# Kernel optimization log

Hardware: AMD Instinct MI355X
Metric: run time of the kernel (lower is better)

The kernel has to match this reference:

```python
import jax, jax.numpy as jnp
import numpy as np

GAMMA = 0.1
BUDGET = 64
EPS = 1e-8  # torch cosine_similarity clamp


def setup_inputs() -> dict:
    key = jax.random.key(0)
    k1, k2, k3, k4 = jax.random.split(key, 4)
    num_nodes, feat_dim, num_cand = 100000, 256, 50000
    return {
        "influence_scores": jax.random.normal(k1, (num_cand,), dtype=jnp.float32),
        "node_features": jax.random.normal(k2, (num_nodes, feat_dim), dtype=jnp.float32),
        "candidate_indices": jax.random.randint(k3, (num_cand,), 0, num_nodes, dtype=jnp.int64),
        "injected_feat": jax.random.normal(k4, (feat_dim,), dtype=jnp.float32),
    }


def reference(influence_scores, node_features, candidate_indices, injected_feat):
    # gather candidate features: [num_cand, feat_dim]
    cand_feat = node_features[candidate_indices]
    # cosine similarity vs injected_feat, torch-style eps clamp on norms
    inj_norm = jnp.maximum(jnp.linalg.norm(injected_feat), EPS)
    cand_norm = jnp.maximum(jnp.linalg.norm(cand_feat, axis=-1), EPS)
    sim_penalty = (cand_feat @ injected_feat) / (cand_norm * inj_norm)
    edge_scores = influence_scores - GAMMA * sim_penalty
    top_k = min(BUDGET, candidate_indices.shape[0])
    _, selected_indices = jax.lax.top_k(edge_scores, top_k)
    return candidate_indices[selected_indices], edge_scores
```

## Files before the change

### kernel.cpp

```cpp
#include <hip/hip_runtime.h>
#include <hip/hip_bf16.h>
#include <float.h>
#include <limits.h>

#define FEAT       256
#define GAMMA_F    0.1f
#define EPS_F      1e-8f
#define KSEL       64
#define NBUCK      8192
#define CAP        4096

__device__ __forceinline__ unsigned key_of(float v) {
    unsigned u = __float_as_uint(v);
    return u ^ ((u >> 31) ? 0xFFFFFFFFu : 0x80000000u);
}

__global__ __launch_bounds__(256) void edge_score_kernel(
    const float* __restrict__ infl,
    const float* __restrict__ feats,
    const int*   __restrict__ cand,
    const float* __restrict__ inj,
    float*       __restrict__ scores,
    int num_cand)
{
    const int gtid = blockIdx.x * blockDim.x + threadIdx.x;
    const int wave = gtid >> 6;
    const int lane = threadIdx.x & 63;
    if (wave >= num_cand) return;

    const int row = cand[wave];
    const float4 f = *reinterpret_cast<const float4*>(
        feats + (size_t)row * FEAT + lane * 4);
    const float4 g = *reinterpret_cast<const float4*>(inj + lane * 4);

    float dot = f.x * g.x + f.y * g.y + f.z * g.z + f.w * g.w;
    float nf  = f.x * f.x + f.y * f.y + f.z * f.z + f.w * f.w;
    float ng  = g.x * g.x + g.y * g.y + g.z * g.z + g.w * g.w;

    #pragma unroll
    for (int off = 32; off > 0; off >>= 1) {
        dot += __shfl_xor(dot, off);
        nf  += __shfl_xor(nf, off);
        ng  += __shfl_xor(ng, off);
    }

    if (lane == 0) {
        const float denom = fmaxf(sqrtf(nf), EPS_F) * fmaxf(sqrtf(ng), EPS_F);
        scores[wave] = infl[wave] - GAMMA_F * (dot / denom);
    }
}

__global__ __launch_bounds__(256) void hist_kernel(
    const float* __restrict__ scores,
    unsigned*    __restrict__ hist,
    int n)
{
    __shared__ unsigned h[NBUCK];
    for (int i = threadIdx.x; i < NBUCK; i += 256) h[i] = 0;
    __syncthreads();
    for (int i = blockIdx.x * 256 + threadIdx.x; i < n; i += gridDim.x * 256)
        atomicAdd(&h[key_of(scores[i]) >> 19], 1u);
    __syncthreads();
    for (int i = threadIdx.x; i < NBUCK; i += 256)
        if (h[i]) atomicAdd(&hist[i], h[i]);
}

__global__ __launch_bounds__(256) void scan_kernel(
    const unsigned* __restrict__ hist,
    unsigned*       __restrict__ meta)
{
    __shared__ unsigned csum[256];
    const int t  = threadIdx.x;
    const int hi = NBUCK - 32 * t;
    unsigned s = 0;
    for (int b = hi - 32; b < hi; ++b) s += hist[b];
    csum[t] = s;
    __syncthreads();

    if (t == 0) {
        unsigned cum = 0;
        int tc = 0;
        for (; tc < 256; ++tc) {
            if (cum + csum[tc] >= KSEL) break;
            cum += csum[tc];
        }
        unsigned B = 0;
        if (tc < 256) {
            int b = NBUCK - 32 * tc - 1;
            for (int k = 0; k < 32; ++k, --b) {
                cum += hist[b];
                if (cum >= KSEL) { B = (unsigned)b; break; }
            }
        }
        meta[0] = B;
    }
}

__global__ __launch_bounds__(256) void compact_kernel(
    const float*    __restrict__ scores,
    const unsigned* __restrict__ meta,
    unsigned*       __restrict__ cnt,
    float*          __restrict__ out_v,
    int*            __restrict__ out_i,
    int n)
{
    const unsigned B = meta[0];
    for (int i = blockIdx.x * 256 + threadIdx.x; i < n; i += gridDim.x * 256) {
        const float v = scores[i];
        if ((key_of(v) >> 19) >= B) {
            const unsigned p = atomicAdd(cnt, 1u);
            if (p < CAP) { out_v[p] = v; out_i[p] = i; }
        }
    }
}

__device__ __forceinline__ bool comes_first(float va, int ia, float vb, int ib) {
    return (va > vb) || (va == vb && ia < ib);
}

__global__ __launch_bounds__(256) void final_kernel(
    const unsigned* __restrict__ cnt,
    const float*    __restrict__ in_v,
    const int*      __restrict__ in_i,
    const int*      __restrict__ cand,
    float*          __restrict__ out)
{
    __shared__ float sv[CAP];
    __shared__ int   si[CAP];
    const int t = threadIdx.x;
    const int m = (int)min(*cnt, (unsigned)CAP);

    if (m <= 256) {
        sv[t] = (t < m) ? in_v[t] : -INFINITY;
        si[t] = (t < m) ? in_i[t] : INT_MAX;
        __syncthreads();
        for (int k = 2; k <= 256; k <<= 1) {
            for (int j = k >> 1; j > 0; j >>= 1) {
                const int p = t ^ j;
                if (p > t) {
                    const float va = sv[t], vb = sv[p];
                    const int   ia = si[t], ib = si[p];
                    const bool asc = ((t & k) == 0);
                    const bool doSwap = asc ? comes_first(vb, ib, va, ia)
                                            : comes_first(va, ia, vb, ib);
                    if (doSwap) { sv[t] = vb; si[t] = ib; sv[p] = va; si[p] = ia; }
                }
                __syncthreads();
            }
        }
        if (t < KSEL) out[t] = (float)cand[si[t]];
        return;
    }

    __shared__ float wv[4];
    __shared__ int   wbi[4], wbs[4];
    for (int i = t; i < CAP; i += 256) {
        sv[i] = (i < m) ? in_v[i] : -INFINITY;
        si[i] = (i < m) ? in_i[i] : INT_MAX;
    }
    __syncthreads();
    for (int k = 0; k < KSEL; ++k) {
        float bv = -INFINITY; int bi = INT_MAX; int bs = 0;
        for (int i = t; i < CAP; i += 256) {
            if (comes_first(sv[i], si[i], bv, bi)) { bv = sv[i]; bi = si[i]; bs = i; }
        }
        #pragma unroll
        for (int off = 32; off > 0; off >>= 1) {
            const float ov = __shfl_xor(bv, off);
            const int   oi = __shfl_xor(bi, off);
            const int   os = __shfl_xor(bs, off);
            if (comes_first(ov, oi, bv, bi)) { bv = ov; bi = oi; bs = os; }
        }
        const int w = t >> 6;
        if ((t & 63) == 0) { wv[w] = bv; wbi[w] = bi; wbs[w] = bs; }
        __syncthreads();
        if (t == 0) {
            float fv = wv[0]; int fi = wbi[0]; int fs = wbs[0];
            #pragma unroll
            for (int j = 1; j < 4; ++j)
                if (comes_first(wv[j], wbi[j], fv, fi)) { fv = wv[j]; fi = wbi[j]; fs = wbs[j]; }
            out[k] = (float)cand[fi];
            sv[fs] = -INFINITY;
            si[fs] = INT_MAX;
        }
        __syncthreads();
    }
}

extern "C" void kernel_launch(void* const* d_in, const int* in_sizes, int n_in,
                              void* d_out, int out_size, void* d_ws, size_t ws_size,
                              hipStream_t stream) {
    const float* infl  = (const float*)d_in[0];
    const float* feats = (const float*)d_in[1];
    const int*   cand  = (const int*)d_in[2];
    const float* inj   = (const float*)d_in[3];

    const int num_cand = in_sizes[0];

    float* out    = (float*)d_out;
    float* scores = (float*)d_out + KSEL;

    unsigned* ws_hist = (unsigned*)d_ws;
    unsigned* ws_cnt  = ws_hist + NBUCK;
    unsigned* ws_meta = ws_cnt + 1;
    float*    ws_v    = (float*)(ws_meta + 1);
    int*      ws_i    = (int*)(ws_v + CAP);

    hipMemsetAsync(ws_hist, 0, (NBUCK + 2) * sizeof(unsigned), stream);

    {
        const int blocks = (num_cand + 3) / 4;
        edge_score_kernel<<<blocks, 256, 0, stream>>>(
            infl, feats, cand, inj, scores, num_cand);
    }

    hist_kernel<<<64, 256, 0, stream>>>(scores, ws_hist, num_cand);

    scan_kernel<<<1, 256, 0, stream>>>(ws_hist, ws_meta);

    compact_kernel<<<64, 256, 0, stream>>>(scores, ws_meta, ws_cnt, ws_v, ws_i, num_cand);

    final_kernel<<<1, 256, 0, stream>>>(ws_cnt, ws_v, ws_i, cand, out);
}
```

Baseline: 49.43 us.

## Fuse histogram into scoring and merge scan/compact/final into one last-block kernel

The histogram update moves into the edge-score kernel as one global atomic per candidate, which removes the separate histogram pass. Scan, compaction and final top-k selection are merged into one 64-block kernel. Each block redundantly scans the histogram, compacts its share, and the last block to finish, detected with an atomic done counter, does the final sort. This cuts launches from five kernels to two, at the cost of 50k contended global atomics on the histogram and a redundant scan in every block.

Result: slower. 141.0 us (+185.2%).

```diff
diff --git a/kernel.cpp b/kernel.cpp
--- a/kernel.cpp
+++ b/kernel.cpp
@@ -9,10 +9,15 @@
 #define KSEL       64
 #define NBUCK      8192
 #define CAP        4096
+#define NB2        64
 
 __device__ __forceinline__ unsigned key_of(float v) {
     unsigned u = __float_as_uint(v);
     return u ^ ((u >> 31) ? 0xFFFFFFFFu : 0x80000000u);
+}
+
+__device__ __forceinline__ bool comes_first(float va, int ia, float vb, int ib) {
+    return (va > vb) || (va == vb && ia < ib);
 }
 
 __global__ __launch_bounds__(256) void edge_score_kernel(
@@ -21,6 +26,7 @@
     const int*   __restrict__ cand,
     const float* __restrict__ inj,
     float*       __restrict__ scores,
+    unsigned*    __restrict__ hist,
     int num_cand)
 {
     const int gtid = blockIdx.x * blockDim.x + threadIdx.x;
@@ -46,37 +52,38 @@
 
     if (lane == 0) {
         const float denom = fmaxf(sqrtf(nf), EPS_F) * fmaxf(sqrtf(ng), EPS_F);
-        scores[wave] = infl[wave] - GAMMA_F * (dot / denom);
-    }
-}
-
-__global__ __launch_bounds__(256) void hist_kernel(
-    const float* __restrict__ scores,
-    unsigned*    __restrict__ hist,
+        const float s = infl[wave] - GAMMA_F * (dot / denom);
+        scores[wave] = s;
+        atomicAdd(&hist[key_of(s) >> 19], 1u);
+    }
+}
+
+__global__ __launch_bounds__(256) void select_kernel(
+    const float*    __restrict__ scores,
+    const unsigned* __restrict__ hist,
+    unsigned*       __restrict__ cnt,
+    unsigned*       __restrict__ done,
+    float*          __restrict__ ws_v,
+    int*            __restrict__ ws_i,
+    const int*      __restrict__ cand,
+    float*          __restrict__ out,
     int n)
 {
-    __shared__ unsigned h[NBUCK];
-    for (int i = threadIdx.x; i < NBUCK; i += 256) h[i] = 0;
-    __syncthreads();
-    for (int i = blockIdx.x * 256 + threadIdx.x; i < n; i += gridDim.x * 256)
-        atomicAdd(&h[key_of(scores[i]) >> 19], 1u);
-    __syncthreads();
-    for (int i = threadIdx.x; i < NBUCK; i += 256)
-        if (h[i]) atomicAdd(&hist[i], h[i]);
-}
-
-__global__ __launch_bounds__(256) void scan_kernel(
-    const unsigned* __restrict__ hist,
-    unsigned*       __restrict__ meta)
-{
     __shared__ unsigned csum[256];
-    const int t  = threadIdx.x;
-    const int hi = NBUCK - 32 * t;
-    unsigned s = 0;
-    for (int b = hi - 32; b < hi; ++b) s += hist[b];
-    csum[t] = s;
-    __syncthreads();
-
+    __shared__ unsigned sB;
+    __shared__ int      sLast;
+    __shared__ float    sv[CAP];
+    __shared__ int      si[CAP];
+
+    const int t = threadIdx.x;
+
+    {
+        const int hi = NBUCK - 32 * t;
+        unsigned s = 0;
+        for (int b = hi - 32; b < hi; ++b) s += hist[b];
+        csum[t] = s;
+    }
+    __syncthreads();
     if (t == 0) {
         unsigned cum = 0;
         int tc = 0;
@@ -92,47 +99,31 @@
                 if (cum >= KSEL) { B = (unsigned)b; break; }
             }
         }
-        meta[0] = B;
-    }
-}
-
-__global__ __launch_bounds__(256) void compact_kernel(
-    const float*    __restrict__ scores,
-    const unsigned* __restrict__ meta,
-    unsigned*       __restrict__ cnt,
-    float*          __restrict__ out_v,
-    int*            __restrict__ out_i,
-    int n)
-{
-    const unsigned B = meta[0];
-    for (int i = blockIdx.x * 256 + threadIdx.x; i < n; i += gridDim.x * 256) {
+        sB = B;
+    }
+    __syncthreads();
+    const unsigned B = sB;
+
+    for (int i = blockIdx.x * 256 + t; i < n; i += NB2 * 256) {
         const float v = scores[i];
         if ((key_of(v) >> 19) >= B) {
             const unsigned p = atomicAdd(cnt, 1u);
-            if (p < CAP) { out_v[p] = v; out_i[p] = i; }
-        }
-    }
-}
-
-__device__ __forceinline__ bool comes_first(float va, int ia, float vb, int ib) {
-    return (va > vb) || (va == vb && ia < ib);
-}
-
-__global__ __launch_bounds__(256) void final_kernel(
-    const unsigned* __restrict__ cnt,
-    const float*    __restrict__ in_v,
-    const int*      __restrict__ in_i,
-    const int*      __restrict__ cand,
-    float*          __restrict__ out)
-{
-    __shared__ float sv[CAP];
-    __shared__ int   si[CAP];
-    const int t = threadIdx.x;
-    const int m = (int)min(*cnt, (unsigned)CAP);
+            if (p < CAP) { ws_v[p] = v; ws_i[p] = i; }
+        }
+    }
+
+    __threadfence();
+    __syncthreads();
+    if (t == 0) sLast = (atomicAdd(done, 1u) == (unsigned)(NB2 - 1));
+    __syncthreads();
+    if (!sLast) return;
+    __threadfence();
+
+    const int m = (int)min(atomicAdd(cnt, 0u), (unsigned)CAP);
 
     if (m <= 256) {
-        sv[t] = (t < m) ? in_v[t] : -INFINITY;
-        si[t] = (t < m) ? in_i[t] : INT_MAX;
+        sv[t] = (t < m) ? ws_v[t] : -INFINITY;
+        si[t] = (t < m) ? ws_i[t] : INT_MAX;
         __syncthreads();
         for (int k = 2; k <= 256; k <<= 1) {
             for (int j = k >> 1; j > 0; j >>= 1) {
@@ -155,8 +146,8 @@
     __shared__ float wv[4];
     __shared__ int   wbi[4], wbs[4];
     for (int i = t; i < CAP; i += 256) {
-        sv[i] = (i < m) ? in_v[i] : -INFINITY;
-        si[i] = (i < m) ? in_i[i] : INT_MAX;
+        sv[i] = (i < m) ? ws_v[i] : -INFINITY;
+        si[i] = (i < m) ? ws_i[i] : INT_MAX;
     }
     __syncthreads();
     for (int k = 0; k < KSEL; ++k) {
@@ -202,8 +193,8 @@
 
     unsigned* ws_hist = (unsigned*)d_ws;
     unsigned* ws_cnt  = ws_hist + NBUCK;
-    unsigned* ws_meta = ws_cnt + 1;
-    float*    ws_v    = (float*)(ws_meta + 1);
+    unsigned* ws_done = ws_cnt + 1;
+    float*    ws_v    = (float*)(ws_done + 1);
     int*      ws_i    = (int*)(ws_v + CAP);
 
     hipMemsetAsync(ws_hist, 0, (NBUCK + 2) * sizeof(unsigned), stream);
@@ -211,14 +202,9 @@
     {
         const int blocks = (num_cand + 3) / 4;
         edge_score_kernel<<<blocks, 256, 0, stream>>>(
-            infl, feats, cand, inj, scores, num_cand);
-    }
-
-    hist_kernel<<<64, 256, 0, stream>>>(scores, ws_hist, num_cand);
-
-    scan_kernel<<<1, 256, 0, stream>>>(ws_hist, ws_meta);
-
-    compact_kernel<<<64, 256, 0, stream>>>(scores, ws_meta, ws_cnt, ws_v, ws_i, num_cand);
-
-    final_kernel<<<1, 256, 0, stream>>>(ws_cnt, ws_v, ws_i, cand, out);
-}
+            infl, feats, cand, inj, scores, ws_hist, num_cand);
+    }
+
+    select_kernel<<<NB2, 256, 0, stream>>>(
+        scores, ws_hist, ws_cnt, ws_done, ws_v, ws_i, cand, out, num_cand);
+}
```
